# Optimization experiments

Hardware: AMD Instinct MI355X
Metric: run time of the kernel (lower is better)

The kernel has to match this reference:

```python
import math
import jax, jax.numpy as jnp
import numpy as np

HID_DIM = 1024
N_HEAD = 16
HEAD_DIM = HID_DIM // N_HEAD
NEG_FILL = -1e9


def _alibi_slopes(n_head: int) -> np.ndarray:
    """ALiBi per-head slopes (Press et al. 2021), matching get_slopes()."""
    main = 2 ** int(math.log2(n_head))
    m = (2.0 ** (-8.0 / main)) ** np.arange(1, 1 + main)
    if main < n_head:
        intra = (2.0 ** (-4.0 / main)) ** np.arange(1, 1 + 2 * (n_head - main), 2)
        m = np.concatenate([m, intra])
    return m.astype(np.float32)  # [H]


def setup_inputs() -> dict:
    key = jax.random.key(0)
    k1, k2, k3 = jax.random.split(key, 3)
    B, S = 2, 2048
    x = jax.random.normal(k1, (B, S, HID_DIM), dtype=jnp.float32)
    mask = jnp.ones((B, S), dtype=jnp.int32)
    Wqkv = jax.random.normal(k2, (HID_DIM, 3 * HID_DIM), dtype=jnp.float32) * 0.02
    Wout = jax.random.normal(k3, (HID_DIM, HID_DIM), dtype=jnp.float32) * 0.02
    return {"x": x, "mask": mask, "Wqkv": Wqkv, "Wout": Wout}


def reference(x, mask, Wqkv, Wout):
    B, S, _ = x.shape
    qkv = x @ Wqkv  # [B,S,3*hid]
    q, k, v = jnp.split(qkv, 3, axis=-1)
    k_cache, v_cache = k, v  # current_cache (pre-reshape, [B,S,hid])

    def to_heads(t):
        return t.reshape(B, S, N_HEAD, HEAD_DIM).transpose(0, 2, 1, 3)  # [B,H,S,Dh]

    q, k, v = to_heads(q), to_heads(k), to_heads(v)

    # NOTE: original code computes self.dk but never scales QK^T by it.
    scores = jnp.einsum('bhqd,bhkd->bhqk', q, k)  # [B,H,S,S]

    # ALiBi bias: tril(j - i), zero on/above diagonal elsewhere per torch.tril
    pos = jnp.arange(S)
    alibi = jnp.tril(pos[None, :] - pos[:, None]).astype(scores.dtype)  # [S,S]
    slopes = jnp.asarray(_alibi_slopes(N_HEAD))  # [H]
    scores = scores + slopes[None, :, None, None] * alibi[None, None]

    # padding mask broadcast over key dim: mask[:,None,None,:]
    scores = jnp.where(mask[:, None, None, :] == 0, NEG_FILL, scores)

    probs = jax.nn.softmax(scores, axis=-1)
    attn = jnp.einsum('bhqk,bhkd->bhqd', probs, v)  # [B,H,S,Dh]
    attn = attn.transpose(0, 2, 1, 3).reshape(B, S, HID_DIM)
    out = attn @ Wout  # dropout is identity in eval / p=0
    return out, k_cache, v_cache
```

## Files before the change

kernel.cpp:

```cpp
#include <hip/hip_runtime.h>
#include <hip/hip_bf16.h>
#include <cstdint>
#include <cstddef>

#define HID 1024
#define NH 16
#define DH 64
#define SEQ 2048
#define BATCH 2
#define BS (BATCH*SEQ)
#define LOG2E 1.4426950408889634f
#define PAD 68

typedef __attribute__((ext_vector_type(8))) short bf16x8;
typedef __attribute__((ext_vector_type(4))) float f32x4;

static __device__ __forceinline__ float fast_exp2(float x) {
    return __builtin_amdgcn_exp2f(x);
}

static __device__ __forceinline__ short f2bf(float f) {
    union { __hip_bfloat16 h; short s; } cv;
    cv.h = __float2bfloat16(f);
    return cv.s;
}
static __device__ __forceinline__ unsigned pack2(float a, float b) {
    union { __hip_bfloat162 h2; unsigned u; } cv;
    cv.h2 = __float22bfloat162_rn(make_float2(a, b));
    return cv.u;
}

typedef const __attribute__((address_space(1))) unsigned gas_u32;
typedef __attribute__((address_space(3))) unsigned las_u32;
static __device__ __forceinline__ void gload_lds16(const short* g, short* l) {
    __builtin_amdgcn_global_load_lds((gas_u32*)g, (las_u32*)l, 16, 0, 0);
}

__global__ __launch_bounds__(256)
void prep(const float* __restrict__ Wqkv, const float* __restrict__ Wout,
          const float* __restrict__ x,
          short* __restrict__ wqkvT, short* __restrict__ woutT,
          short* __restrict__ xb)
{
    __shared__ short tl[64][66];
    const int bid = blockIdx.x;
    const int t = threadIdx.x;

    if (bid >= 1024) {
        const float4* x4 = (const float4*)x;
        uint2* xo = (uint2*)xb;
        const int base = (bid - 1024) * 4096 + t;
        #pragma unroll
        for (int i = 0; i < 16; ++i) {
            float4 f = x4[base + i*256];
            xo[base + i*256] = make_uint2(pack2(f.x, f.y), pack2(f.z, f.w));
        }
        return;
    }

    const float* W; short* WT; int Nw, K, k0, n0;
    if (bid < 768) {
        W = Wqkv; WT = wqkvT; Nw = 3072; K = 1024;
        n0 = (bid % 48) * 64; k0 = (bid / 48) * 64;
    } else {
        W = Wout; WT = woutT; Nw = 1024; K = 1024;
        int b2 = bid - 768;
        n0 = (b2 & 15) * 64; k0 = (b2 >> 4) * 64;
    }
    const int r = t >> 2, c0 = (t & 3) * 16;
    const float* src = W + (size_t)(k0 + r) * Nw + n0 + c0;
    #pragma unroll
    for (int i = 0; i < 16; i += 4) {
        float4 f = *(const float4*)(src + i);
        tl[r][c0+i+0] = f2bf(f.x); tl[r][c0+i+1] = f2bf(f.y);
        tl[r][c0+i+2] = f2bf(f.z); tl[r][c0+i+3] = f2bf(f.w);
    }
    __syncthreads();
    short* dst = WT + (size_t)(n0 + r) * K + k0 + c0;
    unsigned buf[8];
    #pragma unroll
    for (int i = 0; i < 8; ++i) {
        unsigned lo = (unsigned short)tl[c0 + 2*i    ][r];
        unsigned hi = (unsigned short)tl[c0 + 2*i + 1][r];
        buf[i] = lo | (hi << 16);
    }
    *(uint4*)dst       = *(uint4*)&buf[0];
    *((uint4*)dst + 1) = *(uint4*)&buf[4];
}

template<int CMODE, int BN>
__global__ __launch_bounds__(256, 3)
void gemm_lds(const short* __restrict__ A, const short* __restrict__ Bt,
              float* __restrict__ Cf,
              float* __restrict__ kc, float* __restrict__ vc,
              short* __restrict__ qb, short* __restrict__ kb, short* __restrict__ vt,
              int M, int N, int K)
{
    constexpr int WN = BN / 2;
    constexpr int NF = WN / 16;
    __shared__ short As[128*64];
    __shared__ short Bs[BN*64];
    const int t    = threadIdx.x;
    const int wave = t >> 6, lane = t & 63;
    const int quad = lane >> 4, l16 = lane & 15;
    const int wrow = (wave & 1) * 64, wcol = (wave >> 1) * WN;
    const int n0 = blockIdx.x * BN, m0 = blockIdx.y * 128;

    f32x4 acc[4][NF];
    #pragma unroll
    for (int mi = 0; mi < 4; ++mi)
        #pragma unroll
        for (int nj = 0; nj < NF; ++nj) acc[mi][nj] = (f32x4){0.f,0.f,0.f,0.f};

    const int lr = lane >> 3;
    const int lc = (lane & 7) * 8;
    const short* Ab = A  + (size_t)(m0 + wave*32       + lr) * K + lc;
    const short* Bb = Bt + (size_t)(n0 + wave*(BN/4)   + lr) * K + lc;
    short* AsW = As + (wave*32)      * 64;
    short* BsW = Bs + (wave*(BN/4))  * 64;

    for (int kt = 0; kt < K; kt += 64) {
        #pragma unroll
        for (int i = 0; i < 4; ++i)
            gload_lds16(Ab + (size_t)(i*8)*K + kt, AsW + i*512);
        #pragma unroll
        for (int i = 0; i < BN/32; ++i)
            gload_lds16(Bb + (size_t)(i*8)*K + kt, BsW + i*512);
        __syncthreads();

        #pragma unroll
        for (int ks = 0; ks < 2; ++ks) {
            bf16x8 af[4], bfr[NF];
            #pragma unroll
            for (int mi = 0; mi < 4; ++mi)
                af[mi] = *(const bf16x8*)&As[(wrow + mi*16 + l16)*64 + ks*32 + quad*8];
            #pragma unroll
            for (int nj = 0; nj < NF; ++nj)
                bfr[nj] = *(const bf16x8*)&Bs[(wcol + nj*16 + l16)*64 + ks*32 + quad*8];
            #pragma unroll
            for (int mi = 0; mi < 4; ++mi)
                #pragma unroll
                for (int nj = 0; nj < NF; ++nj)
                    acc[mi][nj] = __builtin_amdgcn_mfma_f32_16x16x32_bf16(
                        af[mi], bfr[nj], acc[mi][nj], 0, 0, 0);
        }
        __syncthreads();
    }

    const int region = (CMODE == 0) ? (n0 >> 10) : 0;
    #pragma unroll
    for (int mi = 0; mi < 4; ++mi) {
        int rbase = m0 + wrow + mi*16 + quad*4;
        #pragma unroll
        for (int nj = 0; nj < NF; ++nj) {
            int col = n0 + wcol + nj*16 + l16;
            if (CMODE == 1) {
                #pragma unroll
                for (int reg = 0; reg < 4; ++reg)
                    Cf[(size_t)(rbase + reg) * N + col] = acc[mi][nj][reg];
            } else {
                int c = col & 1023;
                if (region == 0) {
                    #pragma unroll
                    for (int reg = 0; reg < 4; ++reg)
                        qb[(size_t)(rbase + reg) * HID + c] = f2bf(acc[mi][nj][reg] * LOG2E);
                } else if (region == 1) {
                    #pragma unroll
                    for (int reg = 0; reg < 4; ++reg) {
                        float v = acc[mi][nj][reg];
                        kc[(size_t)(rbase + reg) * HID + c] = v;
                        if (kb) kb[(size_t)(rbase + reg) * HID + c] = f2bf(v);
                    }
                } else {
                    #pragma unroll
                    for (int reg = 0; reg < 4; ++reg)
                        vc[(size_t)(rbase + reg) * HID + c] = acc[mi][nj][reg];
                    if (vt) {
                        int b = rbase >> 11, s = rbase & 2047;
                        int h = c >> 6, d = c & 63;
                        unsigned u[2] = {pack2(acc[mi][nj][0], acc[mi][nj][1]),
                                         pack2(acc[mi][nj][2], acc[mi][nj][3])};
                        *(uint2*)&vt[((size_t)((b*16 + h)*64 + d)) * SEQ + s] = *(uint2*)u;
                    }
                }
            }
        }
    }
}

template<bool KVB>
__global__ __launch_bounds__(256, 4)
void attn_kernel(const short* qb,
                 const short* __restrict__ kb, const short* __restrict__ vtg,
                 const float* __restrict__ kc, const float* __restrict__ vc,
                 const int*   __restrict__ mask,
                 short* attn_b)
{
    __shared__ short Ks[64*PAD];
    __shared__ short Vs[64*PAD];
    __shared__ short Ps[64*PAD];
    __shared__ float Mk[64];

    const int t    = threadIdx.x;
    const int wave = t >> 6, lane = t & 63;
    const int quad = lane >> 4, l16 = lane & 15;

    const int blk = blockIdx.x;
    const int qt  = blk & 31;
    const int h   = (blk >> 5) & 15;
    const int b   = blk >> 9;
    const int q0  = qt * 64;
    const float slope2 = exp2f(-0.5f * (float)(h + 1)) * LOG2E;
    const int* mb = mask + b * SEQ;

    const int r  = t >> 2;
    const int c0 = (t & 3) * 16;

    const int qrow0 = q0 + 16*wave + quad*4;

    bf16x8 aq[2];
    #pragma unroll
    for (int ks = 0; ks < 2; ++ks)
        aq[ks] = *(const bf16x8*)(qb + ((size_t)(b*SEQ + q0 + 16*wave + l16)) * HID
                                     + h*DH + ks*32 + quad*8);

    float ls[4];
    f32x4 Oacc[4];
    #pragma unroll
    for (int i = 0; i < 4; ++i) {
        ls[i] = 0.f;
        Oacc[i] = (f32x4){0.f,0.f,0.f,0.f};
    }

    if (KVB) {
        uint4 kr0, kr1, vr0, vr1; float mval = 0.f;
        const short* kbase = kb  + ((size_t)(b*SEQ + r)) * HID + h*DH + c0;
        const short* vbase = vtg + ((size_t)((b*NH + h)*DH + r)) * SEQ + c0;

        kr0 = *(const uint4*)(kbase);
        kr1 = *(const uint4*)(kbase + 8);
        vr0 = *(const uint4*)(vbase);
        vr1 = *(const uint4*)(vbase + 8);
        if (t < 64) mval = (mb[t] == 0) ? -2.0e9f : 0.f;

        for (int kt = 0; kt < 32; ++kt) {
            const int j0 = kt * 64;
            __syncthreads();

            *(uint4*)&Ks[r*PAD + c0]     = kr0;
            *(uint4*)&Ks[r*PAD + c0 + 8] = kr1;
            *(uint4*)&Vs[r*PAD + c0]     = vr0;
            *(uint4*)&Vs[r*PAD + c0 + 8] = vr1;
            if (t < 64) Mk[t] = mval;

            if (kt < 31) {
                const short* kn = kbase + (size_t)(j0 + 64) * HID;
                const short* vn = vbase + (j0 + 64);
                kr0 = *(const uint4*)(kn);
                kr1 = *(const uint4*)(kn + 8);
                vr0 = *(const uint4*)(vn);
                vr1 = *(const uint4*)(vn + 8);
                if (t < 64) mval = (mb[j0 + 64 + t] == 0) ? -2.0e9f : 0.f;
            }
            __syncthreads();

            f32x4 S[4];
            #pragma unroll
            for (int nt = 0; nt < 4; ++nt) S[nt] = (f32x4){0.f,0.f,0.f,0.f};
            #pragma unroll
            for (int ks = 0; ks < 2; ++ks) {
                bf16x8 bk[4];
                #pragma unroll
                for (int nt = 0; nt < 4; ++nt)
                    bk[nt] = *(const bf16x8*)&Ks[(nt*16 + l16)*PAD + ks*32 + quad*8];
                __builtin_amdgcn_s_setprio(1);
                #pragma unroll
                for (int nt = 0; nt < 4; ++nt)
                    S[nt] = __builtin_amdgcn_mfma_f32_16x16x32_bf16(
                        aq[ks], bk[nt], S[nt], 0, 0, 0);
                __builtin_amdgcn_s_setprio(0);
            }

            #pragma unroll
            for (int nt = 0; nt < 4; ++nt) {
                int j = j0 + nt*16 + l16;
                float mn  = Mk[nt*16 + l16];
                float fdb = (float)(j - qrow0);
                float p[4];
                #pragma unroll
                for (int reg = 0; reg < 4; ++reg) {
                    float d = fminf(fdb - (float)reg, 0.f);
                    p[reg] = fast_exp2(fmaf(slope2, d, S[nt][reg]) + mn);
                    ls[reg] += p[reg];
                }
                #pragma unroll
                for (int reg = 0; reg < 4; ++reg)
                    Ps[(16*wave + quad*4 + reg)*PAD + nt*16 + l16] = f2bf(p[reg]);
            }

            #pragma unroll
            for (int ks = 0; ks < 2; ++ks) {
                bf16x8 ap = *(const bf16x8*)&Ps[(16*wave + l16)*PAD + ks*32 + quad*8];
                bf16x8 bv[4];
                #pragma unroll
                for (int nt = 0; nt < 4; ++nt)
                    bv[nt] = *(const bf16x8*)&Vs[(nt*16 + l16)*PAD + ks*32 + quad*8];
                __builtin_amdgcn_s_setprio(1);
                #pragma unroll
                for (int nt = 0; nt < 4; ++nt)
                    Oacc[nt] = __builtin_amdgcn_mfma_f32_16x16x32_bf16(
                        ap, bv[nt], Oacc[nt], 0, 0, 0);
                __builtin_amdgcn_s_setprio(0);
            }
        }
    } else {
        for (int kt = 0; kt < 32; ++kt) {
            const int j0 = kt * 64;
            __syncthreads();
            {
                const float* src = kc + ((size_t)(b*SEQ + j0 + r)) * HID + h*DH + c0;
                #pragma unroll
                for (int i = 0; i < 16; i += 4) {
                    float4 f = *(const float4*)(src + i);
                    *(unsigned*)&Ks[r*PAD + c0 + i]     = pack2(f.x, f.y);
                    *(unsigned*)&Ks[r*PAD + c0 + i + 2] = pack2(f.z, f.w);
                }
                int kp = t & 31, db = t >> 5;
                const float* v0 = vc + ((size_t)(b*SEQ + j0 + 2*kp)) * HID + h*DH + db*8;
                const float* v1 = v0 + HID;
                float4 a0 = *(const float4*)v0, a1 = *(const float4*)(v0 + 4);
                float4 b0 = *(const float4*)v1, b1 = *(const float4*)(v1 + 4);
                float va[8]  = {a0.x,a0.y,a0.z,a0.w,a1.x,a1.y,a1.z,a1.w};
                float vb2[8] = {b0.x,b0.y,b0.z,b0.w,b1.x,b1.y,b1.z,b1.w};
                #pragma unroll
                for (int i = 0; i < 8; ++i)
                    *(unsigned*)&Vs[(db*8 + i)*PAD + 2*kp] = pack2(va[i], vb2[i]);
                if (t < 64) Mk[t] = (mb[j0 + t] == 0) ? -2.0e9f : 0.f;
            }
            __syncthreads();

            f32x4 S[4];
            #pragma unroll
            for (int nt = 0; nt < 4; ++nt) S[nt] = (f32x4){0.f,0.f,0.f,0.f};
            #pragma unroll
            for (int ks = 0; ks < 2; ++ks) {
                bf16x8 bk[4];
                #pragma unroll
                for (int nt = 0; nt < 4; ++nt)
                    bk[nt] = *(const bf16x8*)&Ks[(nt*16 + l16)*PAD + ks*32 + quad*8];
                __builtin_amdgcn_s_setprio(1);
                #pragma unroll
                for (int nt = 0; nt < 4; ++nt)
                    S[nt] = __builtin_amdgcn_mfma_f32_16x16x32_bf16(
                        aq[ks], bk[nt], S[nt], 0, 0, 0);
                __builtin_amdgcn_s_setprio(0);
            }

            #pragma unroll
            for (int nt = 0; nt < 4; ++nt) {
                int j = j0 + nt*16 + l16;
                float mn  = Mk[nt*16 + l16];
                float fdb = (float)(j - qrow0);
                float p[4];
                #pragma unroll
                for (int reg = 0; reg < 4; ++reg) {
                    float d = fminf(fdb - (float)reg, 0.f);
                    p[reg] = fast_exp2(fmaf(slope2, d, S[nt][reg]) + mn);
                    ls[reg] += p[reg];
                }
                #pragma unroll
                for (int reg = 0; reg < 4; ++reg)
                    Ps[(16*wave + quad*4 + reg)*PAD + nt*16 + l16] = f2bf(p[reg]);
            }

            #pragma unroll
            for (int ks = 0; ks < 2; ++ks) {
                bf16x8 ap = *(const bf16x8*)&Ps[(16*wave + l16)*PAD + ks*32 + quad*8];
                bf16x8 bv[4];
                #pragma unroll
                for (int nt = 0; nt < 4; ++nt)
                    bv[nt] = *(const bf16x8*)&Vs[(nt*16 + l16)*PAD + ks*32 + quad*8];
                __builtin_amdgcn_s_setprio(1);
                #pragma unroll
                for (int nt = 0; nt < 4; ++nt)
                    Oacc[nt] = __builtin_amdgcn_mfma_f32_16x16x32_bf16(
                        ap, bv[nt], Oacc[nt], 0, 0, 0);
                __builtin_amdgcn_s_setprio(0);
            }
        }
    }

    float rinv[4];
    #pragma unroll
    for (int reg = 0; reg < 4; ++reg) {
        float s0 = ls[reg];
        #pragma unroll
        for (int off = 1; off <= 8; off <<= 1) s0 += __shfl_xor(s0, off, 64);
        rinv[reg] = 1.0f / s0;
    }

    short* ap = attn_b + (size_t)b * SEQ * HID + h * DH;
    #pragma unroll
    for (int nt = 0; nt < 4; ++nt) {
        int dcol = nt*16 + l16;
        #pragma unroll
        for (int reg = 0; reg < 4; ++reg) {
            int row = q0 + 16*wave + quad*4 + reg;
            ap[(size_t)row * HID + dcol] = f2bf(Oacc[nt][reg] * rinv[reg]);
        }
    }
}

extern "C" void kernel_launch(void* const* d_in, const int* in_sizes, int n_in,
                              void* d_out, int out_size, void* d_ws, size_t ws_size,
                              hipStream_t stream)
{
    const float* x    = (const float*)d_in[0];
    const int*   mask = (const int*)  d_in[1];
    const float* Wqkv = (const float*)d_in[2];
    const float* Wout = (const float*)d_in[3];

    float* out = (float*)d_out;
    float* kc  = out + (size_t)BS * HID;
    float* vc  = kc  + (size_t)BS * HID;

    char*  ws    = (char*)d_ws;
    short* qb    = (short*)ws;
    short* wqkvT = (short*)(ws + (8u << 20));
    short* woutT = (short*)(ws + (14u << 20));
    const bool full = ws_size >= (32u << 20);
    short* kb = full ? (short*)(ws + (16u << 20)) : nullptr;
    short* vt = full ? (short*)(ws + (24u << 20)) : nullptr;

    short* xb = (short*)out;

    prep<<<dim3(1280), dim3(256), 0, stream>>>(Wqkv, Wout, x, wqkvT, woutT, xb);

    gemm_lds<0,128><<<dim3(24, 32), dim3(256), 0, stream>>>(
        xb, wqkvT, nullptr, kc, vc, qb, kb, vt, BS, 3*HID, HID);

    if (full)
        attn_kernel<true><<<dim3(1024), dim3(256), 0, stream>>>(
            qb, kb, vt, kc, vc, mask, qb);
    else
        attn_kernel<false><<<dim3(1024), dim3(256), 0, stream>>>(
            qb, nullptr, nullptr, kc, vc, mask, qb);

    gemm_lds<1,64><<<dim3(16, 32), dim3(256), 0, stream>>>(
        qb, woutT, out, nullptr, nullptr, nullptr, nullptr, nullptr, BS, HID, HID);
}
```

Before: 225.1 us.

## Move V transpose to separate kernel and remap attention blocks per XCD

The strided V-transpose store in the QKV GEMM epilogue is removed. A dedicated vtrans kernel now reads the fp32 V cache through LDS and writes a coalesced bf16 transposed V buffer. The attention grid index is remapped so all query tiles of a given (batch, head) pair land on the same XCD, which should improve L2 reuse of K/V. The fallback attention path also drops its s_setprio hints. The cost is an extra launch and an extra pass over V, in exchange for fewer uncoalesced writes in the GEMM.

```diff
diff --git a/kernel.cpp b/kernel.cpp
--- a/kernel.cpp
+++ b/kernel.cpp
@@ -10,7 +10,7 @@
 #define BATCH 2
 #define BS (BATCH*SEQ)
 #define LOG2E 1.4426950408889634f
-#define PAD 68
+#define PADK 68
 
 typedef __attribute__((ext_vector_type(8))) short bf16x8;
 typedef __attribute__((ext_vector_type(4))) float f32x4;
@@ -88,12 +88,44 @@
     *((uint4*)dst + 1) = *(uint4*)&buf[4];
 }
 
+__global__ __launch_bounds__(256)
+void vtrans(const float* __restrict__ vc, short* __restrict__ vt)
+{
+    __shared__ short tl[64][66];
+    const int bid = blockIdx.x;
+    const int t = threadIdx.x;
+    const int st = bid & 31;
+    const int h  = (bid >> 5) & 15;
+    const int b  = bid >> 9;
+    const int s0 = st * 64;
+
+    const int r = t >> 2, c0 = (t & 3) * 16;
+    const float* src = vc + ((size_t)(b*SEQ + s0 + r)) * HID + h*DH + c0;
+    #pragma unroll
+    for (int i = 0; i < 16; i += 4) {
+        float4 f = *(const float4*)(src + i);
+        tl[r][c0+i+0] = f2bf(f.x); tl[r][c0+i+1] = f2bf(f.y);
+        tl[r][c0+i+2] = f2bf(f.z); tl[r][c0+i+3] = f2bf(f.w);
+    }
+    __syncthreads();
+    short* dst = vt + ((size_t)((b*NH + h)*DH + r)) * SEQ + s0 + c0;
+    unsigned buf[8];
+    #pragma unroll
+    for (int i = 0; i < 8; ++i) {
+        unsigned lo = (unsigned short)tl[c0 + 2*i    ][r];
+        unsigned hi = (unsigned short)tl[c0 + 2*i + 1][r];
+        buf[i] = lo | (hi << 16);
+    }
+    *(uint4*)dst       = *(uint4*)&buf[0];
+    *((uint4*)dst + 1) = *(uint4*)&buf[4];
+}
+
 template<int CMODE, int BN>
 __global__ __launch_bounds__(256, 3)
 void gemm_lds(const short* __restrict__ A, const short* __restrict__ Bt,
               float* __restrict__ Cf,
               float* __restrict__ kc, float* __restrict__ vc,
-              short* __restrict__ qb, short* __restrict__ kb, short* __restrict__ vt,
+              short* __restrict__ qb, short* __restrict__ kb,
               int M, int N, int K)
 {
     constexpr int WN = BN / 2;
@@ -175,13 +207,6 @@
                     #pragma unroll
                     for (int reg = 0; reg < 4; ++reg)
                         vc[(size_t)(rbase + reg) * HID + c] = acc[mi][nj][reg];
-                    if (vt) {
-                        int b = rbase >> 11, s = rbase & 2047;
-                        int h = c >> 6, d = c & 63;
-                        unsigned u[2] = {pack2(acc[mi][nj][0], acc[mi][nj][1]),
-                                         pack2(acc[mi][nj][2], acc[mi][nj][3])};
-                        *(uint2*)&vt[((size_t)((b*16 + h)*64 + d)) * SEQ + s] = *(uint2*)u;
-                    }
                 }
             }
         }
@@ -196,20 +221,23 @@
                  const int*   __restrict__ mask,
                  short* attn_b)
 {
-    __shared__ short Ks[64*PAD];
-    __shared__ short Vs[64*PAD];
-    __shared__ short Ps[64*PAD];
+    __shared__ short Ks[64*PADK];
+    __shared__ short Vs[64*PADK];
+    __shared__ short Ps[64*PADK];
     __shared__ float Mk[64];
 
     const int t    = threadIdx.x;
     const int wave = t >> 6, lane = t & 63;
     const int quad = lane >> 4, l16 = lane & 15;
 
-    const int blk = blockIdx.x;
-    const int qt  = blk & 31;
-    const int h   = (blk >> 5) & 15;
-    const int b   = blk >> 9;
-    const int q0  = qt * 64;
+    const int blk  = blockIdx.x;
+    const int xcd  = blk & 7;
+    const int idx  = blk >> 3;
+    const int pair = xcd * 4 + (idx >> 5);
+    const int qt   = idx & 31;
+    const int h    = pair & 15;
+    const int b    = pair >> 4;
+    const int q0   = qt * 64;
     const float slope2 = exp2f(-0.5f * (float)(h + 1)) * LOG2E;
     const int* mb = mask + b * SEQ;
 
@@ -247,10 +275,10 @@
             const int j0 = kt * 64;
             __syncthreads();
 
-            *(uint4*)&Ks[r*PAD + c0]     = kr0;
-            *(uint4*)&Ks[r*PAD + c0 + 8] = kr1;
-            *(uint4*)&Vs[r*PAD + c0]     = vr0;
-            *(uint4*)&Vs[r*PAD + c0 + 8] = vr1;
+            *(uint4*)&Ks[r*PADK + c0]     = kr0;
+            *(uint4*)&Ks[r*PADK + c0 + 8] = kr1;
+            *(uint4*)&Vs[r*PADK + c0]     = vr0;
+            *(uint4*)&Vs[r*PADK + c0 + 8] = vr1;
             if (t < 64) Mk[t] = mval;
 
             if (kt < 31) {
@@ -272,7 +300,7 @@
                 bf16x8 bk[4];
                 #pragma unroll
                 for (int nt = 0; nt < 4; ++nt)
-                    bk[nt] = *(const bf16x8*)&Ks[(nt*16 + l16)*PAD + ks*32 + quad*8];
+                    bk[nt] = *(const bf16x8*)&Ks[(nt*16 + l16)*PADK + ks*32 + quad*8];
                 __builtin_amdgcn_s_setprio(1);
                 #pragma unroll
                 for (int nt = 0; nt < 4; ++nt)
@@ -295,16 +323,16 @@
                 }
                 #pragma unroll
                 for (int reg = 0; reg < 4; ++reg)
-                    Ps[(16*wave + quad*4 + reg)*PAD + nt*16 + l16] = f2bf(p[reg]);
+                    Ps[(16*wave + quad*4 + reg)*PADK + nt*16 + l16] = f2bf(p[reg]);
             }
 
             #pragma unroll
             for (int ks = 0; ks < 2; ++ks) {
-                bf16x8 ap = *(const bf16x8*)&Ps[(16*wave + l16)*PAD + ks*32 + quad*8];
+                bf16x8 ap = *(const bf16x8*)&Ps[(16*wave + l16)*PADK + ks*32 + quad*8];
                 bf16x8 bv[4];
                 #pragma unroll
                 for (int nt = 0; nt < 4; ++nt)
-                    bv[nt] = *(const bf16x8*)&Vs[(nt*16 + l16)*PAD + ks*32 + quad*8];
+                    bv[nt] = *(const bf16x8*)&Vs[(nt*16 + l16)*PADK + ks*32 + quad*8];
                 __builtin_amdgcn_s_setprio(1);
                 #pragma unroll
                 for (int nt = 0; nt < 4; ++nt)
@@ -322,8 +350,8 @@
                 #pragma unroll
                 for (int i = 0; i < 16; i += 4) {
                     float4 f = *(const float4*)(src + i);
-                    *(unsigned*)&Ks[r*PAD + c0 + i]     = pack2(f.x, f.y);
-                    *(unsigned*)&Ks[r*PAD + c0 + i + 2] = pack2(f.z, f.w);
+                    *(unsigned*)&Ks[r*PADK + c0 + i]     = pack2(f.x, f.y);
+                    *(unsigned*)&Ks[r*PADK + c0 + i + 2] = pack2(f.z, f.w);
                 }
                 int kp = t & 31, db = t >> 5;
                 const float* v0 = vc + ((size_t)(b*SEQ + j0 + 2*kp)) * HID + h*DH + db*8;
@@ -334,7 +362,7 @@
                 float vb2[8] = {b0.x,b0.y,b0.z,b0.w,b1.x,b1.y,b1.z,b1.w};
                 #pragma unroll
                 for (int i = 0; i < 8; ++i)
-                    *(unsigned*)&Vs[(db*8 + i)*PAD + 2*kp] = pack2(va[i], vb2[i]);
+                    *(unsigned*)&Vs[(db*8 + i)*PADK + 2*kp] = pack2(va[i], vb2[i]);
                 if (t < 64) Mk[t] = (mb[j0 + t] == 0) ? -2.0e9f : 0.f;
             }
             __syncthreads();
@@ -347,13 +375,11 @@
                 bf16x8 bk[4];
                 #pragma unroll
                 for (int nt = 0; nt < 4; ++nt)
-                    bk[nt] = *(const bf16x8*)&Ks[(nt*16 + l16)*PAD + ks*32 + quad*8];
-                __builtin_amdgcn_s_setprio(1);
+                    bk[nt] = *(const bf16x8*)&Ks[(nt*16 + l16)*PADK + ks*32 + quad*8];
                 #pragma unroll
                 for (int nt = 0; nt < 4; ++nt)
                     S[nt] = __builtin_amdgcn_mfma_f32_16x16x32_bf16(
                         aq[ks], bk[nt], S[nt], 0, 0, 0);
-                __builtin_amdgcn_s_setprio(0);
             }
 
             #pragma unroll
@@ -370,22 +396,20 @@
                 }
                 #pragma unroll
                 for (int reg = 0; reg < 4; ++reg)
-                    Ps[(16*wave + quad*4 + reg)*PAD + nt*16 + l16] = f2bf(p[reg]);
+                    Ps[(16*wave + quad*4 + reg)*PADK + nt*16 + l16] = f2bf(p[reg]);
             }
 
             #pragma unroll
             for (int ks = 0; ks < 2; ++ks) {
-                bf16x8 ap = *(const bf16x8*)&Ps[(16*wave + l16)*PAD + ks*32 + quad*8];
+                bf16x8 ap = *(const bf16x8*)&Ps[(16*wave + l16)*PADK + ks*32 + quad*8];
                 bf16x8 bv[4];
                 #pragma unroll
                 for (int nt = 0; nt < 4; ++nt)
-                    bv[nt] = *(const bf16x8*)&Vs[(nt*16 + l16)*PAD + ks*32 + quad*8];
-                __builtin_amdgcn_s_setprio(1);
+                    bv[nt] = *(const bf16x8*)&Vs[(nt*16 + l16)*PADK + ks*32 + quad*8];
                 #pragma unroll
                 for (int nt = 0; nt < 4; ++nt)
                     Oacc[nt] = __builtin_amdgcn_mfma_f32_16x16x32_bf16(
                         ap, bv[nt], Oacc[nt], 0, 0, 0);
-                __builtin_amdgcn_s_setprio(0);
             }
         }
     }
@@ -437,15 +461,17 @@
     prep<<<dim3(1280), dim3(256), 0, stream>>>(Wqkv, Wout, x, wqkvT, woutT, xb);
 
     gemm_lds<0,128><<<dim3(24, 32), dim3(256), 0, stream>>>(
-        xb, wqkvT, nullptr, kc, vc, qb, kb, vt, BS, 3*HID, HID);
-
-    if (full)
+        xb, wqkvT, nullptr, kc, vc, qb, kb, BS, 3*HID, HID);
+
+    if (full) {
+        vtrans<<<dim3(1024), dim3(256), 0, stream>>>(vc, vt);
         attn_kernel<true><<<dim3(1024), dim3(256), 0, stream>>>(
             qb, kb, vt, kc, vc, mask, qb);
-    else
+    } else {
         attn_kernel<false><<<dim3(1024), dim3(256), 0, stream>>>(
             qb, nullptr, nullptr, kc, vc, mask, qb);
+    }
 
     gemm_lds<1,64><<<dim3(16, 32), dim3(256), 0, stream>>>(
-        qb, woutT, out, nullptr, nullptr, nullptr, nullptr, nullptr, BS, HID, HID);
-}
+        qb, woutT, out, nullptr, nullptr, nullptr, nullptr, BS, HID, HID);
+}
```

After: 230.4 us. 2.4% more time.
